# Kernel tuning notes

Measured on AMD Instinct MI355X. Metric: run time of the kernel, lower is better.

The kernel has to match this reference:

```python
import jax, jax.numpy as jnp
import numpy as np

N_NODES = 50000
FEAT_DIM = 256
HIDDEN = 64
CLASS_DIM = 64
N_EDGES = 800000
K_HOPS = 2


def setup_inputs() -> dict:
    key = jax.random.key(0)
    k1, k2, k3, k4, k5, k6 = jax.random.split(key, 6)
    x = jax.random.normal(k1, (N_NODES, FEAT_DIM), dtype=jnp.float32)
    edge_rows = jax.random.randint(k2, (N_EDGES,), 0, N_NODES, dtype=jnp.int32)
    edge_cols = jax.random.randint(k3, (N_EDGES,), 0, N_NODES, dtype=jnp.int32)
    edge_vals = jax.random.uniform(k4, (N_EDGES,), dtype=jnp.float32)  # normalized-adj values (>0)
    # xavier_uniform-style init scale
    lim_e = float(np.sqrt(6.0 / (FEAT_DIM + HIDDEN)))
    lim_c = float(np.sqrt(6.0 / (7 * HIDDEN + CLASS_DIM)))
    w_embed = jax.random.uniform(k5, (FEAT_DIM, HIDDEN), dtype=jnp.float32, minval=-lim_e, maxval=lim_e)
    w_classify = jax.random.uniform(k6, (7 * HIDDEN, CLASS_DIM), dtype=jnp.float32, minval=-lim_c, maxval=lim_c)
    return {"x": x, "edge_rows": edge_rows, "edge_cols": edge_cols,
            "edge_vals": edge_vals, "w_embed": w_embed, "w_classify": w_classify}


def reference(x, edge_rows, edge_cols, edge_vals, w_embed, w_classify):
    # Node_GCN forward (eval mode; dropout inert).
    # a1 = adj - I, a2 = adj@adj - adj - I  =>
    #   a1 @ r = s - r,   a2 @ r = adj@s - s - r   with s = adj @ r
    n = x.shape[0]

    def spmm(r):  # adj @ r via edge-list gather + segment-sum: [n, d]
        return jax.ops.segment_sum(edge_vals[:, None] * r[edge_cols], edge_rows, num_segments=n)

    act = jax.nn.relu
    r = act(x @ w_embed)                  # [n, h]
    rs = [r]
    for _ in range(K_HOPS):
        s = spmm(r)                       # adj @ r
        t = spmm(s)                       # adj @ adj @ r
        r1 = s - r                        # a1 @ r
        r2 = t - s - r                    # a2 @ r
        r = act(jnp.concatenate([r1, r2], axis=1))  # width doubles each hop
        rs.append(r)
    r_final = jnp.concatenate(rs, axis=1)  # [n, 7h]
    return jax.nn.softmax(r_final @ w_classify, axis=1)
```

## Files before the change

### kernel.cpp

```cpp
#include <hip/hip_runtime.h>

#define N_NODES 50000
#define NPAD 50048
#define FEAT 256
#define HID 64
#define NEDGE 800000
#define SCAN_CHUNK 2048
#define NB_SCAN 25

typedef unsigned short bf16_t;
typedef __attribute__((ext_vector_type(8))) short bf16x8;
typedef __attribute__((ext_vector_type(4))) float f32x4;

#define MFMA_BF16 __builtin_amdgcn_mfma_f32_16x16x32_bf16

__device__ __forceinline__ float bf2f(bf16_t b) {
    union { unsigned u; float f; } v; v.u = ((unsigned)b) << 16; return v.f;
}
__device__ __forceinline__ bf16_t f2bf(float f) {
    union { float f; unsigned u; } v; v.f = f;
    unsigned r = v.u + 0x7fff + ((v.u >> 16) & 1);
    return (bf16_t)(r >> 16);
}
__device__ __forceinline__ void unpack2(unsigned u, float& lo, float& hi) {
    union { unsigned u; float f; } a, b;
    a.u = u << 16; b.u = u & 0xffff0000u;
    lo = a.f; hi = b.f;
}
__device__ __forceinline__ unsigned pack2(float lo, float hi) {
    return ((unsigned)f2bf(lo)) | (((unsigned)f2bf(hi)) << 16);
}

__global__ __launch_bounds__(256) void pack_w_kernel(const float* __restrict__ wsrc,
        bf16_t* __restrict__ wdst, int nkstep) {
    int idx = blockIdx.x * 256 + threadIdx.x;
    if (idx >= nkstep * 256) return;
    int lane = idx & 63, nt = (idx >> 6) & 3, ks = idx >> 8;
    int kb  = ks * 32 + ((lane >> 4) * 8);
    int col = nt * 16 + (lane & 15);
    unsigned p[4];
#pragma unroll
    for (int j = 0; j < 4; ++j)
        p[j] = pack2(wsrc[(size_t)(kb + 2*j) * 64 + col],
                     wsrc[(size_t)(kb + 2*j + 1) * 64 + col]);
    uint4 u; u.x = p[0]; u.y = p[1]; u.z = p[2]; u.w = p[3];
    *(uint4*)(wdst + (size_t)idx * 8) = u;
}

__global__ __launch_bounds__(256) void embed_mfma(const float* __restrict__ x,
        const bf16_t* __restrict__ wep, bf16_t* __restrict__ r0) {
    const int t = threadIdx.x;
    const int l = t & 63, w = t >> 6;
    const int lm = l & 15, lg = l >> 4;
    const int base = blockIdx.x * 128 + w * 32;

    int m0 = base + lm, m1 = base + 16 + lm;
    if (m0 >= N_NODES) m0 = N_NODES - 1;
    if (m1 >= N_NODES) m1 = N_NODES - 1;
    const float* xp0 = x + (size_t)m0 * FEAT + lg * 8;
    const float* xp1 = x + (size_t)m1 * FEAT + lg * 8;

    f32x4 acc[2][4];
#pragma unroll
    for (int i = 0; i < 2; ++i)
#pragma unroll
        for (int j = 0; j < 4; ++j) acc[i][j] = (f32x4){0.f, 0.f, 0.f, 0.f};

    auto aload = [&](const float* p) {
        float4 u0 = *(const float4*)(p);
        float4 u1 = *(const float4*)(p + 4);
        bf16x8 r;
        r[0] = (short)f2bf(u0.x); r[1] = (short)f2bf(u0.y);
        r[2] = (short)f2bf(u0.z); r[3] = (short)f2bf(u0.w);
        r[4] = (short)f2bf(u1.x); r[5] = (short)f2bf(u1.y);
        r[6] = (short)f2bf(u1.z); r[7] = (short)f2bf(u1.w);
        return r;
    };
    auto wb = [&](int ks, int nt) {
        return *(const bf16x8*)(wep + ((size_t)(ks * 4 + nt) * 64 + l) * 8);
    };

    const int NK = FEAT / 32;
    bf16x8 a0 = aload(xp0), a1 = aload(xp1);
    bf16x8 b0 = wb(0,0), b1 = wb(0,1), b2 = wb(0,2), b3 = wb(0,3);
    for (int ks = 0; ks < NK; ++ks) {
        bf16x8 na0, na1, nb0, nb1, nb2, nb3;
        const bool more = (ks + 1 < NK);
        if (more) {
            int kt = (ks + 1) * 32;
            na0 = aload(xp0 + kt); na1 = aload(xp1 + kt);
            nb0 = wb(ks+1,0); nb1 = wb(ks+1,1); nb2 = wb(ks+1,2); nb3 = wb(ks+1,3);
        }
        acc[0][0] = MFMA_BF16(a0, b0, acc[0][0], 0, 0, 0);
        acc[1][0] = MFMA_BF16(a1, b0, acc[1][0], 0, 0, 0);
        acc[0][1] = MFMA_BF16(a0, b1, acc[0][1], 0, 0, 0);
        acc[1][1] = MFMA_BF16(a1, b1, acc[1][1], 0, 0, 0);
        acc[0][2] = MFMA_BF16(a0, b2, acc[0][2], 0, 0, 0);
        acc[1][2] = MFMA_BF16(a1, b2, acc[1][2], 0, 0, 0);
        acc[0][3] = MFMA_BF16(a0, b3, acc[0][3], 0, 0, 0);
        acc[1][3] = MFMA_BF16(a1, b3, acc[1][3], 0, 0, 0);
        if (more) { a0 = na0; a1 = na1; b0 = nb0; b1 = nb1; b2 = nb2; b3 = nb3; }
    }

#pragma unroll
    for (int rt = 0; rt < 2; ++rt)
#pragma unroll
        for (int r = 0; r < 4; ++r) {
            int R = base + rt * 16 + lg * 4 + r;
            if (R < N_NODES) {
                bf16_t* o = r0 + (size_t)R * HID + lm;
                o[0]  = f2bf(fmaxf(acc[rt][0][r], 0.f));
                o[16] = f2bf(fmaxf(acc[rt][1][r], 0.f));
                o[32] = f2bf(fmaxf(acc[rt][2][r], 0.f));
                o[48] = f2bf(fmaxf(acc[rt][3][r], 0.f));
            }
        }
}

__global__ __launch_bounds__(256) void hist_kernel(const int* __restrict__ rows,
        int* __restrict__ cnt) {
    int e = blockIdx.x * 256 + threadIdx.x;
    if (e < NEDGE) atomicAdd(&cnt[rows[e]], 1);
}

__global__ __launch_bounds__(256) void scan_a(const int* __restrict__ cnt,
        int* __restrict__ bsum) {
    __shared__ int sd[256];
    const int t = threadIdx.x;
    const int base = blockIdx.x * SCAN_CHUNK + t * 8;
    int s = 0;
#pragma unroll
    for (int i = 0; i < 8; ++i) {
        int idx = base + i;
        s += (idx < N_NODES) ? cnt[idx] : 0;
    }
    sd[t] = s; __syncthreads();
    for (int off = 128; off > 0; off >>= 1) {
        if (t < off) sd[t] += sd[t + off];
        __syncthreads();
    }
    if (t == 0) bsum[blockIdx.x] = sd[0];
}

__global__ __launch_bounds__(64) void scan_b(int* __restrict__ bsum,
        int* __restrict__ rowPtr) {
    if (threadIdx.x == 0) {
        int run = 0;
        for (int b = 0; b < NB_SCAN; ++b) {
            int v = bsum[b];
            bsum[b] = run;
            run += v;
        }
        rowPtr[N_NODES] = run;
    }
}

__global__ __launch_bounds__(256) void scan_c(const int* __restrict__ cnt,
        const int* __restrict__ boff, int* __restrict__ rowPtr) {
    __shared__ int sd[256];
    const int t = threadIdx.x;
    const int base = blockIdx.x * SCAN_CHUNK + t * 8;
    int v[8];
    int s = 0;
#pragma unroll
    for (int i = 0; i < 8; ++i) {
        int idx = base + i;
        v[i] = (idx < N_NODES) ? cnt[idx] : 0;
        s += v[i];
    }
    sd[t] = s; __syncthreads();
    for (int off = 1; off < 256; off <<= 1) {
        int add = (t >= off) ? sd[t - off] : 0;
        __syncthreads();
        sd[t] += add;
        __syncthreads();
    }
    int run = boff[blockIdx.x] + (sd[t] - s);
#pragma unroll
    for (int i = 0; i < 8; ++i) {
        int idx = base + i;
        if (idx < N_NODES) rowPtr[idx] = run;
        run += v[i];
    }
}

__global__ __launch_bounds__(256) void scatter_kernel(const int* __restrict__ rows,
        const int* __restrict__ cols, const float* __restrict__ vals,
        const int* __restrict__ rowPtr, int* __restrict__ fill,
        uint2* __restrict__ colval) {
    int e = blockIdx.x * 256 + threadIdx.x;
    if (e < NEDGE) {
        int r = rows[e];
        int p = rowPtr[r] + atomicAdd(&fill[r], 1);
        uint2 cv; cv.x = (unsigned)cols[e]; cv.y = __float_as_uint(vals[e]);
        colval[p] = cv;
    }
}

__global__ __launch_bounds__(256) void spmm64_kernel(const uint2* __restrict__ colval,
        const int* __restrict__ rowPtr,
        const bf16_t* __restrict__ src, bf16_t* __restrict__ dst) {
    const int lane = threadIdx.x & 63;
    const int row  = (int)((blockIdx.x * 256u + threadIdx.x) >> 6);
    const int beg = rowPtr[row], end = rowPtr[row + 1];
    float acc = 0.f;
    int i = beg;
    for (; i + 8 <= end; i += 8) {
        uint2 cv[8]; float g[8];
#pragma unroll
        for (int j = 0; j < 8; ++j) cv[j] = colval[i+j];
#pragma unroll
        for (int j = 0; j < 8; ++j) g[j] = bf2f(src[(size_t)cv[j].x*HID + lane]);
#pragma unroll
        for (int j = 0; j < 8; ++j) acc += __uint_as_float(cv[j].y)*g[j];
    }
    for (; i < end; ++i) {
        uint2 cv = colval[i];
        acc += __uint_as_float(cv.y) * bf2f(src[(size_t)cv.x*HID + lane]);
    }
    dst[(size_t)row*HID + lane] = f2bf(acc);
}

__global__ __launch_bounds__(256) void spmm64f_kernel(const uint2* __restrict__ colval,
        const int* __restrict__ rowPtr,
        const bf16_t* __restrict__ s, const bf16_t* __restrict__ r0,
        bf16_t* __restrict__ r1c) {
    const int lane = threadIdx.x & 63;
    const int row  = (int)((blockIdx.x * 256u + threadIdx.x) >> 6);
    const int beg = rowPtr[row], end = rowPtr[row + 1];
    float acc = 0.f;
    int i = beg;
    for (; i + 8 <= end; i += 8) {
        uint2 cv[8]; float g[8];
#pragma unroll
        for (int j = 0; j < 8; ++j) cv[j] = colval[i+j];
#pragma unroll
        for (int j = 0; j < 8; ++j) g[j] = bf2f(s[(size_t)cv[j].x*HID + lane]);
#pragma unroll
        for (int j = 0; j < 8; ++j) acc += __uint_as_float(cv[j].y)*g[j];
    }
    for (; i < end; ++i) {
        uint2 cv = colval[i];
        acc += __uint_as_float(cv.y) * bf2f(s[(size_t)cv.x*HID + lane]);
    }
    float sv = bf2f(s[(size_t)row*HID + lane]);
    float rv = bf2f(r0[(size_t)row*HID + lane]);
    r1c[(size_t)row*128 + lane]      = f2bf(fmaxf(sv - rv, 0.f));
    r1c[(size_t)row*128 + 64 + lane] = f2bf(fmaxf(acc - sv - rv, 0.f));
}

__global__ __launch_bounds__(256) void spmm128_kernel(const uint2* __restrict__ colval,
        const int* __restrict__ rowPtr,
        const bf16_t* __restrict__ src, bf16_t* __restrict__ dst) {
    const int lane = threadIdx.x & 63;
    const int row  = (int)((blockIdx.x * 256u + threadIdx.x) >> 6);
    const int beg = rowPtr[row], end = rowPtr[row + 1];
    const unsigned* srcu = (const unsigned*)src;
    float a0 = 0.f, a1 = 0.f;
    int i = beg;
    for (; i + 4 <= end; i += 4) {
        uint2 cv[4]; unsigned u[4];
#pragma unroll
        for (int j = 0; j < 4; ++j) cv[j] = colval[i+j];
#pragma unroll
        for (int j = 0; j < 4; ++j) u[j] = srcu[(size_t)cv[j].x*64 + lane];
#pragma unroll
        for (int j = 0; j < 4; ++j) {
            float lo, hi; unpack2(u[j], lo, hi);
            float v = __uint_as_float(cv[j].y);
            a0 += v*lo; a1 += v*hi;
        }
    }
    for (; i < end; ++i) {
        uint2 cv = colval[i];
        float lo, hi; unpack2(srcu[(size_t)cv.x*64 + lane], lo, hi);
        float v = __uint_as_float(cv.y);
        a0 += v*lo; a1 += v*hi;
    }
    ((unsigned*)dst)[(size_t)row*64 + lane] = pack2(a0, a1);
}

__global__ __launch_bounds__(256) void spmm128f_kernel(const uint2* __restrict__ colval,
        const int* __restrict__ rowPtr,
        const bf16_t* __restrict__ s2, const bf16_t* __restrict__ r1,
        bf16_t* __restrict__ r2c) {
    const int lane = threadIdx.x & 63;
    const int row  = (int)((blockIdx.x * 256u + threadIdx.x) >> 6);
    const int beg = rowPtr[row], end = rowPtr[row + 1];
    const unsigned* s2u = (const unsigned*)s2;
    const unsigned* r1u = (const unsigned*)r1;
    float a0 = 0.f, a1 = 0.f;
    int i = beg;
    for (; i + 4 <= end; i += 4) {
        uint2 cv[4]; unsigned u[4];
#pragma unroll
        for (int j = 0; j < 4; ++j) cv[j] = colval[i+j];
#pragma unroll
        for (int j = 0; j < 4; ++j) u[j] = s2u[(size_t)cv[j].x*64 + lane];
#pragma unroll
        for (int j = 0; j < 4; ++j) {
            float lo, hi; unpack2(u[j], lo, hi);
            float v = __uint_as_float(cv[j].y);
            a0 += v*lo; a1 += v*hi;
        }
    }
    for (; i < end; ++i) {
        uint2 cv = colval[i];
        float lo, hi; unpack2(s2u[(size_t)cv.x*64 + lane], lo, hi);
        float v = __uint_as_float(cv.y);
        a0 += v*lo; a1 += v*hi;
    }
    float s0v, s1v, r0v, r1v;
    unpack2(s2u[(size_t)row*64 + lane], s0v, s1v);
    unpack2(r1u[(size_t)row*64 + lane], r0v, r1v);
    unsigned* r2u = (unsigned*)r2c;
    r2u[(size_t)row*128 + lane]      = pack2(fmaxf(s0v - r0v, 0.f), fmaxf(s1v - r1v, 0.f));
    r2u[(size_t)row*128 + 64 + lane] = pack2(fmaxf(a0 - s0v - r0v, 0.f), fmaxf(a1 - s1v - r1v, 0.f));
}

__global__ __launch_bounds__(256) void classify_mfma(const bf16_t* __restrict__ r0,
        const bf16_t* __restrict__ r1, const bf16_t* __restrict__ r2,
        const bf16_t* __restrict__ wcp, float* __restrict__ out) {
    const int t = threadIdx.x;
    const int l = t & 63, w = t >> 6;
    const int lm = l & 15, lg = l >> 4;
    const int base = blockIdx.x * 128 + w * 32;

    const int m0 = base + lm, m1 = base + 16 + lm;
    const bf16_t* p0_r0 = r0 + (size_t)m0 * 64  + lg * 8;
    const bf16_t* p0_r1 = r1 + (size_t)m0 * 128 + lg * 8;
    const bf16_t* p0_r2 = r2 + (size_t)m0 * 256 + lg * 8;
    const bf16_t* p1_r0 = r0 + (size_t)m1 * 64  + lg * 8;
    const bf16_t* p1_r1 = r1 + (size_t)m1 * 128 + lg * 8;
    const bf16_t* p1_r2 = r2 + (size_t)m1 * 256 + lg * 8;

    f32x4 acc[2][4];
#pragma unroll
    for (int i = 0; i < 2; ++i)
#pragma unroll
        for (int j = 0; j < 4; ++j) acc[i][j] = (f32x4){0.f, 0.f, 0.f, 0.f};

    auto aload = [&](const bf16_t* pr0, const bf16_t* pr1, const bf16_t* pr2, int kt) {
        const bf16_t* p = (kt < 64) ? (pr0 + kt) : (kt < 192) ? (pr1 + kt - 64) : (pr2 + kt - 192);
        return *(const bf16x8*)p;
    };
    auto wb = [&](int ks, int nt) {
        return *(const bf16x8*)(wcp + ((size_t)(ks * 4 + nt) * 64 + l) * 8);
    };

    const int NK = 14;
    bf16x8 a0 = aload(p0_r0, p0_r1, p0_r2, 0);
    bf16x8 a1 = aload(p1_r0, p1_r1, p1_r2, 0);
    bf16x8 b0 = wb(0,0), b1 = wb(0,1), b2 = wb(0,2), b3 = wb(0,3);
    for (int ks = 0; ks < NK; ++ks) {
        bf16x8 na0, na1, nb0, nb1, nb2, nb3;
        const bool more = (ks + 1 < NK);
        if (more) {
            int kt = (ks + 1) * 32;
            na0 = aload(p0_r0, p0_r1, p0_r2, kt);
            na1 = aload(p1_r0, p1_r1, p1_r2, kt);
            nb0 = wb(ks+1,0); nb1 = wb(ks+1,1); nb2 = wb(ks+1,2); nb3 = wb(ks+1,3);
        }
        acc[0][0] = MFMA_BF16(a0, b0, acc[0][0], 0, 0, 0);
        acc[1][0] = MFMA_BF16(a1, b0, acc[1][0], 0, 0, 0);
        acc[0][1] = MFMA_BF16(a0, b1, acc[0][1], 0, 0, 0);
        acc[1][1] = MFMA_BF16(a1, b1, acc[1][1], 0, 0, 0);
        acc[0][2] = MFMA_BF16(a0, b2, acc[0][2], 0, 0, 0);
        acc[1][2] = MFMA_BF16(a1, b2, acc[1][2], 0, 0, 0);
        acc[0][3] = MFMA_BF16(a0, b3, acc[0][3], 0, 0, 0);
        acc[1][3] = MFMA_BF16(a1, b3, acc[1][3], 0, 0, 0);
        if (more) { a0 = na0; a1 = na1; b0 = nb0; b1 = nb1; b2 = nb2; b3 = nb3; }
    }

#pragma unroll
    for (int rt = 0; rt < 2; ++rt)
#pragma unroll
        for (int r = 0; r < 4; ++r) {
            float v0 = acc[rt][0][r], v1 = acc[rt][1][r];
            float v2 = acc[rt][2][r], v3 = acc[rt][3][r];
            float m = fmaxf(fmaxf(v0, v1), fmaxf(v2, v3));
#pragma unroll
            for (int o = 1; o < 16; o <<= 1) m = fmaxf(m, __shfl_xor(m, o));
            float e0 = __expf(v0 - m), e1 = __expf(v1 - m);
            float e2 = __expf(v2 - m), e3 = __expf(v3 - m);
            float s = e0 + e1 + e2 + e3;
#pragma unroll
            for (int o = 1; o < 16; o <<= 1) s += __shfl_xor(s, o);
            float inv = 1.f / s;
            int R = base + rt * 16 + lg * 4 + r;
            if (R < N_NODES) {
                float* o = out + (size_t)R * 64 + lm;
                o[0]  = e0 * inv;
                o[16] = e1 * inv;
                o[32] = e2 * inv;
                o[48] = e3 * inv;
            }
        }
}

extern "C" void kernel_launch(void* const* d_in, const int* in_sizes, int n_in,
                              void* d_out, int out_size, void* d_ws, size_t ws_size,
                              hipStream_t stream) {
    const float* x    = (const float*)d_in[0];
    const int*   erow = (const int*)d_in[1];
    const int*   ecol = (const int*)d_in[2];
    const float* eval = (const float*)d_in[3];
    const float* we   = (const float*)d_in[4];
    const float* wc   = (const float*)d_in[5];
    float* out = (float*)d_out;

    char* wsp = (char*)d_ws;
    size_t off = 0;
    auto take = [&](size_t bytes) {
        char* p = wsp + off;
        off += (bytes + 255) & ~(size_t)255;
        return p;
    };
    bf16_t* r0     = (bf16_t*)take((size_t)NPAD * 64 * 2);
    bf16_t* sbuf   = (bf16_t*)take((size_t)NPAD * 128 * 2);
    bf16_t* r1c    = (bf16_t*)take((size_t)NPAD * 128 * 2);
    bf16_t* r2c    = (bf16_t*)take((size_t)NPAD * 256 * 2);
    int*    cnt    = (int*)take((size_t)N_NODES * 4);
    int*    rowPtr = (int*)take((size_t)(N_NODES + 1) * 4);
    int*    fill   = (int*)take((size_t)N_NODES * 4);
    int*    bsum   = (int*)take((size_t)NB_SCAN * 4);
    uint2*  colval = (uint2*)take((size_t)NEDGE * 8);
    bf16_t* wep    = (bf16_t*)take((size_t)8  * 256 * 8 * 2);
    bf16_t* wcp    = (bf16_t*)take((size_t)14 * 256 * 8 * 2);
    (void)ws_size; (void)in_sizes; (void)n_in; (void)out_size;

    hipMemsetAsync(cnt,  0, (size_t)N_NODES * 4, stream);
    hipMemsetAsync(fill, 0, (size_t)N_NODES * 4, stream);

    pack_w_kernel<<<8,  256, 0, stream>>>(we, wep, 8);
    pack_w_kernel<<<14, 256, 0, stream>>>(wc, wcp, 14);

    embed_mfma<<<NPAD / 128, 256, 0, stream>>>(x, wep, r0);

    hist_kernel<<<3125, 256, 0, stream>>>(erow, cnt);
    scan_a<<<NB_SCAN, 256, 0, stream>>>(cnt, bsum);
    scan_b<<<1, 64, 0, stream>>>(bsum, rowPtr);
    scan_c<<<NB_SCAN, 256, 0, stream>>>(cnt, bsum, rowPtr);
    scatter_kernel<<<3125, 256, 0, stream>>>(erow, ecol, eval, rowPtr, fill, colval);

    spmm64_kernel <<<12500, 256, 0, stream>>>(colval, rowPtr, r0, sbuf);
    spmm64f_kernel<<<12500, 256, 0, stream>>>(colval, rowPtr, sbuf, r0, r1c);
    spmm128_kernel<<<12500, 256, 0, stream>>>(colval, rowPtr, r1c, sbuf);
    spmm128f_kernel<<<12500, 256, 0, stream>>>(colval, rowPtr, sbuf, r1c, r2c);

    classify_mfma<<<NPAD / 128, 256, 0, stream>>>(r0, r1c, r2c, wcp, out);
}
```

Before: 277.2 us.

## Build CSR via two-level bucket sort, fuse scan stages, unroll spmm128 gathers by 8

Replaces the per-row global-atomic scatter with a two-pass build. Edges are first binned into 128-row buckets using few global atomics, then each bucket is sorted into CSR order with LDS atomics and a scan. The single-thread scan_b kernel is folded into scan_c, removing one launch. The 128-wide SpMM gather loops are unrolled to 8 edges to keep more loads in flight. This adds an extra temporary pass over the edges and more workspace, and it changes the order of edges within a row.

```diff
diff --git a/kernel.cpp b/kernel.cpp
--- a/kernel.cpp
+++ b/kernel.cpp
@@ -7,6 +7,8 @@
 #define NEDGE 800000
 #define SCAN_CHUNK 2048
 #define NB_SCAN 25
+#define RPB 128
+#define NBKT 391
 
 typedef unsigned short bf16_t;
 typedef __attribute__((ext_vector_type(8))) short bf16x8;
@@ -142,24 +144,22 @@
     if (t == 0) bsum[blockIdx.x] = sd[0];
 }
 
-__global__ __launch_bounds__(64) void scan_b(int* __restrict__ bsum,
-        int* __restrict__ rowPtr) {
-    if (threadIdx.x == 0) {
-        int run = 0;
+__global__ __launch_bounds__(256) void scan_c(const int* __restrict__ cnt,
+        const int* __restrict__ bsum, int* __restrict__ rowPtr) {
+    __shared__ int sd[256];
+    __shared__ int sboff;
+    const int t = threadIdx.x;
+    const int base = blockIdx.x * SCAN_CHUNK + t * 8;
+    if (t == 0) {
+        int a = 0, tot = 0;
         for (int b = 0; b < NB_SCAN; ++b) {
             int v = bsum[b];
-            bsum[b] = run;
-            run += v;
-        }
-        rowPtr[N_NODES] = run;
-    }
-}
-
-__global__ __launch_bounds__(256) void scan_c(const int* __restrict__ cnt,
-        const int* __restrict__ boff, int* __restrict__ rowPtr) {
-    __shared__ int sd[256];
-    const int t = threadIdx.x;
-    const int base = blockIdx.x * SCAN_CHUNK + t * 8;
+            if (b < (int)blockIdx.x) a += v;
+            tot += v;
+        }
+        sboff = a;
+        if (blockIdx.x == NB_SCAN - 1) rowPtr[N_NODES] = tot;
+    }
     int v[8];
     int s = 0;
 #pragma unroll
@@ -175,7 +175,7 @@
         sd[t] += add;
         __syncthreads();
     }
-    int run = boff[blockIdx.x] + (sd[t] - s);
+    int run = sboff + (sd[t] - s);
 #pragma unroll
     for (int i = 0; i < 8; ++i) {
         int idx = base + i;
@@ -184,16 +184,53 @@
     }
 }
 
-__global__ __launch_bounds__(256) void scatter_kernel(const int* __restrict__ rows,
+__global__ __launch_bounds__(256) void bin_kernel(const int* __restrict__ rows,
         const int* __restrict__ cols, const float* __restrict__ vals,
-        const int* __restrict__ rowPtr, int* __restrict__ fill,
-        uint2* __restrict__ colval) {
+        const int* __restrict__ rowPtr, int* __restrict__ bfill,
+        int* __restrict__ tmpR, uint2* __restrict__ tmpCV) {
     int e = blockIdx.x * 256 + threadIdx.x;
     if (e < NEDGE) {
         int r = rows[e];
-        int p = rowPtr[r] + atomicAdd(&fill[r], 1);
+        int b = r >> 7;
+        int p = rowPtr[b << 7] + atomicAdd(&bfill[b], 1);
+        tmpR[p] = r;
         uint2 cv; cv.x = (unsigned)cols[e]; cv.y = __float_as_uint(vals[e]);
-        colval[p] = cv;
+        tmpCV[p] = cv;
+    }
+}
+
+__global__ __launch_bounds__(256) void bucket_csr_kernel(const int* __restrict__ rowPtr,
+        const int* __restrict__ tmpR, const uint2* __restrict__ tmpCV,
+        uint2* __restrict__ colval) {
+    __shared__ int cnt[RPB];
+    __shared__ int off[RPB];
+    const int t = threadIdx.x;
+    const int b = blockIdx.x;
+    const int r0 = b << 7;
+    const int r1 = (r0 + RPB < N_NODES) ? (r0 + RPB) : N_NODES;
+    const int base = rowPtr[r0];
+    const int nE = rowPtr[r1] - base;
+
+    if (t < RPB) cnt[t] = 0;
+    __syncthreads();
+    for (int i = t; i < nE; i += 256)
+        atomicAdd(&cnt[tmpR[base + i] - r0], 1);
+    __syncthreads();
+    if (t < RPB) off[t] = cnt[t];
+    __syncthreads();
+    for (int d = 1; d < RPB; d <<= 1) {
+        int v = 0;
+        if (t < RPB && t >= d) v = off[t - d];
+        __syncthreads();
+        if (t < RPB) off[t] += v;
+        __syncthreads();
+    }
+    if (t < RPB) off[t] -= cnt[t];
+    __syncthreads();
+    for (int i = t; i < nE; i += 256) {
+        int r = tmpR[base + i];
+        int p = atomicAdd(&off[r - r0], 1);
+        colval[base + p] = tmpCV[base + i];
     }
 }
 
@@ -258,14 +295,14 @@
     const unsigned* srcu = (const unsigned*)src;
     float a0 = 0.f, a1 = 0.f;
     int i = beg;
-    for (; i + 4 <= end; i += 4) {
-        uint2 cv[4]; unsigned u[4];
-#pragma unroll
-        for (int j = 0; j < 4; ++j) cv[j] = colval[i+j];
-#pragma unroll
-        for (int j = 0; j < 4; ++j) u[j] = srcu[(size_t)cv[j].x*64 + lane];
-#pragma unroll
-        for (int j = 0; j < 4; ++j) {
+    for (; i + 8 <= end; i += 8) {
+        uint2 cv[8]; unsigned u[8];
+#pragma unroll
+        for (int j = 0; j < 8; ++j) cv[j] = colval[i+j];
+#pragma unroll
+        for (int j = 0; j < 8; ++j) u[j] = srcu[(size_t)cv[j].x*64 + lane];
+#pragma unroll
+        for (int j = 0; j < 8; ++j) {
             float lo, hi; unpack2(u[j], lo, hi);
             float v = __uint_as_float(cv[j].y);
             a0 += v*lo; a1 += v*hi;
@@ -291,14 +328,14 @@
     const unsigned* r1u = (const unsigned*)r1;
     float a0 = 0.f, a1 = 0.f;
     int i = beg;
-    for (; i + 4 <= end; i += 4) {
-        uint2 cv[4]; unsigned u[4];
-#pragma unroll
-        for (int j = 0; j < 4; ++j) cv[j] = colval[i+j];
-#pragma unroll
-        for (int j = 0; j < 4; ++j) u[j] = s2u[(size_t)cv[j].x*64 + lane];
-#pragma unroll
-        for (int j = 0; j < 4; ++j) {
+    for (; i + 8 <= end; i += 8) {
+        uint2 cv[8]; unsigned u[8];
+#pragma unroll
+        for (int j = 0; j < 8; ++j) cv[j] = colval[i+j];
+#pragma unroll
+        for (int j = 0; j < 8; ++j) u[j] = s2u[(size_t)cv[j].x*64 + lane];
+#pragma unroll
+        for (int j = 0; j < 8; ++j) {
             float lo, hi; unpack2(u[j], lo, hi);
             float v = __uint_as_float(cv[j].y);
             a0 += v*lo; a1 += v*hi;
@@ -422,15 +459,17 @@
     bf16_t* r2c    = (bf16_t*)take((size_t)NPAD * 256 * 2);
     int*    cnt    = (int*)take((size_t)N_NODES * 4);
     int*    rowPtr = (int*)take((size_t)(N_NODES + 1) * 4);
-    int*    fill   = (int*)take((size_t)N_NODES * 4);
+    int*    bfill  = (int*)take((size_t)NBKT * 4);
     int*    bsum   = (int*)take((size_t)NB_SCAN * 4);
     uint2*  colval = (uint2*)take((size_t)NEDGE * 8);
+    int*    tmpR   = (int*)take((size_t)NEDGE * 4);
+    uint2*  tmpCV  = (uint2*)take((size_t)NEDGE * 8);
     bf16_t* wep    = (bf16_t*)take((size_t)8  * 256 * 8 * 2);
     bf16_t* wcp    = (bf16_t*)take((size_t)14 * 256 * 8 * 2);
     (void)ws_size; (void)in_sizes; (void)n_in; (void)out_size;
 
-    hipMemsetAsync(cnt,  0, (size_t)N_NODES * 4, stream);
-    hipMemsetAsync(fill, 0, (size_t)N_NODES * 4, stream);
+    hipMemsetAsync(cnt,   0, (size_t)N_NODES * 4, stream);
+    hipMemsetAsync(bfill, 0, (size_t)NBKT * 4, stream);
 
     pack_w_kernel<<<8,  256, 0, stream>>>(we, wep, 8);
     pack_w_kernel<<<14, 256, 0, stream>>>(wc, wcp, 14);
@@ -439,9 +478,9 @@
 
     hist_kernel<<<3125, 256, 0, stream>>>(erow, cnt);
     scan_a<<<NB_SCAN, 256, 0, stream>>>(cnt, bsum);
-    scan_b<<<1, 64, 0, stream>>>(bsum, rowPtr);
     scan_c<<<NB_SCAN, 256, 0, stream>>>(cnt, bsum, rowPtr);
-    scatter_kernel<<<3125, 256, 0, stream>>>(erow, ecol, eval, rowPtr, fill, colval);
+    bin_kernel<<<3125, 256, 0, stream>>>(erow, ecol, eval, rowPtr, bfill, tmpR, tmpCV);
+    bucket_csr_kernel<<<NBKT, 256, 0, stream>>>(rowPtr, tmpR, tmpCV, colval);
 
     spmm64_kernel <<<12500, 256, 0, stream>>>(colval, rowPtr, r0, sbuf);
     spmm64f_kernel<<<12500, 256, 0, stream>>>(colval, rowPtr, sbuf, r0, r1c);
```

Result: slower. 530.1 us (+91.2%).

## Merge preprocessing kernels to cut launches and fold scan offsets into scan_c

Applied to the files above, without the earlier changes.

Merges the histogram and both weight-packing launches into one prep kernel. Removes the serial scan_b launch by having each scan_c block sum the block totals itself, and zeroes the fill counters in scan_c instead of with a separate memset. Fuses the CSR scatter with the embedding GEMM in one grid, so the atomic-heavy scatter and the MFMA GEMM run side by side. This cuts launch count and idle gaps at the cost of heterogeneous blocks and slight redundant work in scan_c.

```diff
diff --git a/kernel.cpp b/kernel.cpp
--- a/kernel.cpp
+++ b/kernel.cpp
@@ -7,6 +7,8 @@
 #define NEDGE 800000
 #define SCAN_CHUNK 2048
 #define NB_SCAN 25
+#define NB_EDGE 3125
+#define NB_GEMM 391
 
 typedef unsigned short bf16_t;
 typedef __attribute__((ext_vector_type(8))) short bf16x8;
@@ -31,10 +33,8 @@
     return ((unsigned)f2bf(lo)) | (((unsigned)f2bf(hi)) << 16);
 }
 
-__global__ __launch_bounds__(256) void pack_w_kernel(const float* __restrict__ wsrc,
-        bf16_t* __restrict__ wdst, int nkstep) {
-    int idx = blockIdx.x * 256 + threadIdx.x;
-    if (idx >= nkstep * 256) return;
+__device__ __forceinline__ void pack_w_body(const float* __restrict__ wsrc,
+        bf16_t* __restrict__ wdst, int idx) {
     int lane = idx & 63, nt = (idx >> 6) & 3, ks = idx >> 8;
     int kb  = ks * 32 + ((lane >> 4) * 8);
     int col = nt * 16 + (lane & 15);
@@ -47,12 +47,101 @@
     *(uint4*)(wdst + (size_t)idx * 8) = u;
 }
 
-__global__ __launch_bounds__(256) void embed_mfma(const float* __restrict__ x,
-        const bf16_t* __restrict__ wep, bf16_t* __restrict__ r0) {
+__global__ __launch_bounds__(256) void prep_kernel(const int* __restrict__ rows,
+        int* __restrict__ cnt, const float* __restrict__ we, bf16_t* __restrict__ wep,
+        const float* __restrict__ wc, bf16_t* __restrict__ wcp) {
+    const int b = blockIdx.x, t = threadIdx.x;
+    if (b < NB_EDGE) {
+        int e = b * 256 + t;
+        if (e < NEDGE) atomicAdd(&cnt[rows[e]], 1);
+    } else if (b < NB_EDGE + 8) {
+        pack_w_body(we, wep, (b - NB_EDGE) * 256 + t);
+    } else {
+        pack_w_body(wc, wcp, (b - NB_EDGE - 8) * 256 + t);
+    }
+}
+
+__global__ __launch_bounds__(256) void scan_a(const int* __restrict__ cnt,
+        int* __restrict__ bsum) {
+    __shared__ int sd[256];
+    const int t = threadIdx.x;
+    const int base = blockIdx.x * SCAN_CHUNK + t * 8;
+    int s = 0;
+#pragma unroll
+    for (int i = 0; i < 8; ++i) {
+        int idx = base + i;
+        s += (idx < N_NODES) ? cnt[idx] : 0;
+    }
+    sd[t] = s; __syncthreads();
+    for (int off = 128; off > 0; off >>= 1) {
+        if (t < off) sd[t] += sd[t + off];
+        __syncthreads();
+    }
+    if (t == 0) bsum[blockIdx.x] = sd[0];
+}
+
+__global__ __launch_bounds__(256) void scan_c(const int* __restrict__ cnt,
+        const int* __restrict__ bsum, int* __restrict__ rowPtr,
+        int* __restrict__ fill) {
+    __shared__ int sd[256];
+    __shared__ int sboff;
+    const int t = threadIdx.x;
+    const int base = blockIdx.x * SCAN_CHUNK + t * 8;
+    if (t == 0) {
+        int a = 0, tot = 0;
+        for (int b = 0; b < NB_SCAN; ++b) {
+            int v = bsum[b];
+            if (b < (int)blockIdx.x) a += v;
+            tot += v;
+        }
+        sboff = a;
+        if (blockIdx.x == NB_SCAN - 1) rowPtr[N_NODES] = tot;
+    }
+    int v[8];
+    int s = 0;
+#pragma unroll
+    for (int i = 0; i < 8; ++i) {
+        int idx = base + i;
+        v[i] = (idx < N_NODES) ? cnt[idx] : 0;
+        s += v[i];
+    }
+    sd[t] = s; __syncthreads();
+    for (int off = 1; off < 256; off <<= 1) {
+        int add = (t >= off) ? sd[t - off] : 0;
+        __syncthreads();
+        sd[t] += add;
+        __syncthreads();
+    }
+    int run = sboff + (sd[t] - s);
+#pragma unroll
+    for (int i = 0; i < 8; ++i) {
+        int idx = base + i;
+        if (idx < N_NODES) { rowPtr[idx] = run; fill[idx] = 0; }
+        run += v[i];
+    }
+}
+
+__global__ __launch_bounds__(256) void scatter_embed_kernel(
+        const int* __restrict__ rows, const int* __restrict__ cols,
+        const float* __restrict__ vals, const int* __restrict__ rowPtr,
+        int* __restrict__ fill, uint2* __restrict__ colval,
+        const float* __restrict__ x, const bf16_t* __restrict__ wep,
+        bf16_t* __restrict__ r0) {
+    if (blockIdx.x < NB_EDGE) {
+        int e = blockIdx.x * 256 + threadIdx.x;
+        if (e < NEDGE) {
+            int r = rows[e];
+            int p = rowPtr[r] + atomicAdd(&fill[r], 1);
+            uint2 cv; cv.x = (unsigned)cols[e]; cv.y = __float_as_uint(vals[e]);
+            colval[p] = cv;
+        }
+        return;
+    }
+    const int blk = blockIdx.x - NB_EDGE;
     const int t = threadIdx.x;
     const int l = t & 63, w = t >> 6;
     const int lm = l & 15, lg = l >> 4;
-    const int base = blockIdx.x * 128 + w * 32;
+    const int base = blk * 128 + w * 32;
 
     int m0 = base + lm, m1 = base + 16 + lm;
     if (m0 >= N_NODES) m0 = N_NODES - 1;
@@ -115,86 +204,6 @@
                 o[48] = f2bf(fmaxf(acc[rt][3][r], 0.f));
             }
         }
-}
-
-__global__ __launch_bounds__(256) void hist_kernel(const int* __restrict__ rows,
-        int* __restrict__ cnt) {
-    int e = blockIdx.x * 256 + threadIdx.x;
-    if (e < NEDGE) atomicAdd(&cnt[rows[e]], 1);
-}
-
-__global__ __launch_bounds__(256) void scan_a(const int* __restrict__ cnt,
-        int* __restrict__ bsum) {
-    __shared__ int sd[256];
-    const int t = threadIdx.x;
-    const int base = blockIdx.x * SCAN_CHUNK + t * 8;
-    int s = 0;
-#pragma unroll
-    for (int i = 0; i < 8; ++i) {
-        int idx = base + i;
-        s += (idx < N_NODES) ? cnt[idx] : 0;
-    }
-    sd[t] = s; __syncthreads();
-    for (int off = 128; off > 0; off >>= 1) {
-        if (t < off) sd[t] += sd[t + off];
-        __syncthreads();
-    }
-    if (t == 0) bsum[blockIdx.x] = sd[0];
-}
-
-__global__ __launch_bounds__(64) void scan_b(int* __restrict__ bsum,
-        int* __restrict__ rowPtr) {
-    if (threadIdx.x == 0) {
-        int run = 0;
-        for (int b = 0; b < NB_SCAN; ++b) {
-            int v = bsum[b];
-            bsum[b] = run;
-            run += v;
-        }
-        rowPtr[N_NODES] = run;
-    }
-}
-
-__global__ __launch_bounds__(256) void scan_c(const int* __restrict__ cnt,
-        const int* __restrict__ boff, int* __restrict__ rowPtr) {
-    __shared__ int sd[256];
-    const int t = threadIdx.x;
-    const int base = blockIdx.x * SCAN_CHUNK + t * 8;
-    int v[8];
-    int s = 0;
-#pragma unroll
-    for (int i = 0; i < 8; ++i) {
-        int idx = base + i;
-        v[i] = (idx < N_NODES) ? cnt[idx] : 0;
-        s += v[i];
-    }
-    sd[t] = s; __syncthreads();
-    for (int off = 1; off < 256; off <<= 1) {
-        int add = (t >= off) ? sd[t - off] : 0;
-        __syncthreads();
-        sd[t] += add;
-        __syncthreads();
-    }
-    int run = boff[blockIdx.x] + (sd[t] - s);
-#pragma unroll
-    for (int i = 0; i < 8; ++i) {
-        int idx = base + i;
-        if (idx < N_NODES) rowPtr[idx] = run;
-        run += v[i];
-    }
-}
-
-__global__ __launch_bounds__(256) void scatter_kernel(const int* __restrict__ rows,
-        const int* __restrict__ cols, const float* __restrict__ vals,
-        const int* __restrict__ rowPtr, int* __restrict__ fill,
-        uint2* __restrict__ colval) {
-    int e = blockIdx.x * 256 + threadIdx.x;
-    if (e < NEDGE) {
-        int r = rows[e];
-        int p = rowPtr[r] + atomicAdd(&fill[r], 1);
-        uint2 cv; cv.x = (unsigned)cols[e]; cv.y = __float_as_uint(vals[e]);
-        colval[p] = cv;
-    }
 }
 
 __global__ __launch_bounds__(256) void spmm64_kernel(const uint2* __restrict__ colval,
@@ -429,24 +438,18 @@
     bf16_t* wcp    = (bf16_t*)take((size_t)14 * 256 * 8 * 2);
     (void)ws_size; (void)in_sizes; (void)n_in; (void)out_size;
 
-    hipMemsetAsync(cnt,  0, (size_t)N_NODES * 4, stream);
-    hipMemsetAsync(fill, 0, (size_t)N_NODES * 4, stream);
-
-    pack_w_kernel<<<8,  256, 0, stream>>>(we, wep, 8);
-    pack_w_kernel<<<14, 256, 0, stream>>>(wc, wcp, 14);
-
-    embed_mfma<<<NPAD / 128, 256, 0, stream>>>(x, wep, r0);
-
-    hist_kernel<<<3125, 256, 0, stream>>>(erow, cnt);
+    hipMemsetAsync(cnt, 0, (size_t)N_NODES * 4, stream);
+
+    prep_kernel<<<NB_EDGE + 8 + 14, 256, 0, stream>>>(erow, cnt, we, wep, wc, wcp);
     scan_a<<<NB_SCAN, 256, 0, stream>>>(cnt, bsum);
-    scan_b<<<1, 64, 0, stream>>>(bsum, rowPtr);
-    scan_c<<<NB_SCAN, 256, 0, stream>>>(cnt, bsum, rowPtr);
-    scatter_kernel<<<3125, 256, 0, stream>>>(erow, ecol, eval, rowPtr, fill, colval);
+    scan_c<<<NB_SCAN, 256, 0, stream>>>(cnt, bsum, rowPtr, fill);
+    scatter_embed_kernel<<<NB_EDGE + NB_GEMM, 256, 0, stream>>>(
+        erow, ecol, eval, rowPtr, fill, colval, x, wep, r0);
 
     spmm64_kernel <<<12500, 256, 0, stream>>>(colval, rowPtr, r0, sbuf);
     spmm64f_kernel<<<12500, 256, 0, stream>>>(colval, rowPtr, sbuf, r0, r1c);
     spmm128_kernel<<<12500, 256, 0, stream>>>(colval, rowPtr, r1c, sbuf);
     spmm128f_kernel<<<12500, 256, 0, stream>>>(colval, rowPtr, sbuf, r1c, r2c);
 
-    classify_mfma<<<NPAD / 128, 256, 0, stream>>>(r0, r1c, r2c, wcp, out);
-}
+    classify_mfma<<<NB_GEMM, 256, 0, stream>>>(r0, r1c, r2c, wcp, out);
+}
```

New measurement: 274.4 us. No clear change (-1.0%).
